# Optimization experiments

Hardware: AMD Instinct MI355X
Metric: run time of the kernel (lower is better)

## Reference

```python
import jax, jax.numpy as jnp
import numpy as np

OUT_F, IN_F = 4096, 4096
TOKENS = 8192


def setup_inputs() -> dict:
    key = jax.random.key(0)
    k0, k1, k2, k3 = jax.random.split(key, 4)
    CORE_SCALE = 0.05  # keep reconstructed W finite and well below the 1e6 sanity bound
    x = jax.random.normal(k0, (TOKENS, IN_F), dtype=jnp.float32)
    core0 = jax.random.normal(k1, (1, 16, 16, 64), dtype=jnp.float32) * CORE_SCALE
    core1 = jax.random.normal(k2, (64, 16, 16, 64), dtype=jnp.float32) * CORE_SCALE
    core2 = jax.random.normal(k3, (64, 16, 16, 1), dtype=jnp.float32) * CORE_SCALE
    return {"x": x, "core0": core0, "core1": core1, "core2": core2}


def _build_weight(cores):
    # Chain tensordot over bond dims: cores[k] is [r_{k-1}, o_k, i_k, r_k]
    t = cores[0].astype(jnp.float32)
    for c in cores[1:]:
        t = jnp.tensordot(t, c.astype(jnp.float32), axes=((-1,), (0,)))
    # squeeze the boundary bonds (both 1 for open boundary)
    t = t[0, ..., 0]  # shape [o1, i1, o2, i2, o3, i3]
    num = len(cores)
    # order 'oi': all o-axes first, then all i-axes (matches _contract_4d_chain_with)
    perm = list(range(0, 2 * num, 2)) + list(range(1, 2 * num, 2))
    t = jnp.transpose(t, perm)
    W = t.reshape(OUT_F, IN_F)
    # _clean_finite: nan/inf -> 0 (identity on finite values)
    return jnp.nan_to_num(W, nan=0.0, posinf=0.0, neginf=0.0)


def reference(x, core0, core1, core2):
    W = _build_weight([core0, core1, core2])  # [out_f, in_f], fp32
    # dense path: y = x @ W^T (nn.Linear semantics, no bias)
    return jnp.matmul(x, W.T)
```

## Files before the change

kernel.cpp:

```cpp
#include <hip/hip_runtime.h>

typedef __attribute__((ext_vector_type(8))) short  s8v;
typedef __attribute__((ext_vector_type(8))) unsigned short us8;
typedef __attribute__((ext_vector_type(4))) unsigned short us4;
typedef __attribute__((ext_vector_type(4))) float  f4v;

__device__ __forceinline__ unsigned short f2bf(float f) {
  unsigned int u = __builtin_bit_cast(unsigned int, f);
  u += 0x7fffu + ((u >> 16) & 1u);
  return (unsigned short)(u >> 16);
}

__device__ __forceinline__ void gll16(const void* g, void* l) {
  __builtin_amdgcn_global_load_lds(
      (const __attribute__((address_space(1))) unsigned int*)g,
      (__attribute__((address_space(3))) unsigned int*)l, 16, 0, 0);
}

__global__ __launch_bounds__(256) void cast_bf16(const float* __restrict__ in,
                                                 unsigned short* __restrict__ out) {
  const size_t i = (size_t)blockIdx.x * 256 + threadIdx.x;
  const f4v* p = (const f4v*)in;
  f4v a = p[2 * i];
  f4v b = p[2 * i + 1];
  us8 r;
  r[0] = f2bf(a[0]); r[1] = f2bf(a[1]); r[2] = f2bf(a[2]); r[3] = f2bf(a[3]);
  r[4] = f2bf(b[0]); r[5] = f2bf(b[1]); r[6] = f2bf(b[2]); r[7] = f2bf(b[3]);
  *(us8*)&out[i * 8] = r;
}

__global__ __launch_bounds__(256) void contract1b(const float* __restrict__ c0,
                                                  const float* __restrict__ c1,
                                                  unsigned short* __restrict__ T) {
  const int idx = blockIdx.x * 256 + threadIdx.x;
  const int r2q = idx & 15;
  const int oi2 = (idx >> 4) & 255;
  const int oi1 = idx >> 12;
  const float* c0p = c0 + oi1 * 64;
  const float* c1p = c1 + oi2 * 64 + r2q * 4;
  f4v s = (f4v)0.f;
#pragma unroll 8
  for (int r1 = 0; r1 < 64; ++r1) {
    const float t = c0p[r1];
    const f4v v = *(const f4v*)(c1p + r1 * 16384);
    s[0] = fmaf(t, v[0], s[0]); s[1] = fmaf(t, v[1], s[1]);
    s[2] = fmaf(t, v[2], s[2]); s[3] = fmaf(t, v[3], s[3]);
  }
  us4 o;
  o[0] = f2bf(s[0]); o[1] = f2bf(s[1]); o[2] = f2bf(s[2]); o[3] = f2bf(s[3]);
  *(us4*)&T[(size_t)idx * 4] = o;
}

__global__ __launch_bounds__(256) void transc2(const float* __restrict__ c2,
                                               unsigned short* __restrict__ c2t) {
  const int n = blockIdx.x * 16 + (threadIdx.x >> 4);
  const int j = threadIdx.x & 15;
  us4 o;
#pragma unroll
  for (int q = 0; q < 4; ++q) o[q] = f2bf(c2[(j * 4 + q) * 256 + n]);
  *(us4*)&c2t[(size_t)n * 64 + j * 4] = o;
}

__global__ __launch_bounds__(256) void buildW3(const unsigned short* __restrict__ T,
                                               const unsigned short* __restrict__ c2t,
                                               unsigned short* __restrict__ W) {
  __shared__ unsigned short sT[16384];
  __shared__ unsigned short sC[16384];

  const int tid = threadIdx.x;
  const int o1 = blockIdx.x >> 4, o2 = blockIdx.x & 15;

#pragma unroll
  for (int j = 0; j < 8; ++j) {
    const int c = j * 256 + tid;
    const int m = c >> 3, sl = c & 7;
    const int dst = m * 64 + ((sl ^ (m & 7)) << 3);
    *(us8*)&sT[dst] = *(const us8*)(T + (size_t)(o1 * 16 + (m >> 4)) * 16384 +
                                    (o2 * 16 + (m & 15)) * 64 + sl * 8);
    *(us8*)&sC[dst] = *(const us8*)(c2t + (size_t)m * 64 + sl * 8);
  }
  __syncthreads();

  const int lane = tid & 63, wid = tid >> 6;
  const int fr = lane & 15, ks = lane >> 4;
  const int f7 = fr & 7;
  const int sx0 = ((ks ^ f7) << 3);
  const int sx1 = (((4 + ks) ^ f7) << 3);

  s8v a[4][2];
#pragma unroll
  for (int mi = 0; mi < 4; ++mi) {
    const unsigned short* p = &sT[(wid * 64 + mi * 16 + fr) * 64];
    a[mi][0] = *(const s8v*)(p + sx0);
    a[mi][1] = *(const s8v*)(p + sx1);
  }
#pragma unroll
  for (int nt = 0; nt < 16; ++nt) {
    const unsigned short* p = &sC[(nt * 16 + fr) * 64];
    const s8v b0 = *(const s8v*)(p + sx0);
    const s8v b1 = *(const s8v*)(p + sx1);
#pragma unroll
    for (int mi = 0; mi < 4; ++mi) {
      f4v acc = (f4v)0.f;
      acc = __builtin_amdgcn_mfma_f32_16x16x32_bf16(a[mi][0], b0, acc, 0, 0, 0);
      acc = __builtin_amdgcn_mfma_f32_16x16x32_bf16(a[mi][1], b1, acc, 0, 0, 0);
      unsigned short* wp = W + (size_t)(o1 * 256 + o2 * 16 + nt) * 4096 +
                           (wid * 4 + mi) * 256 + fr;
#pragma unroll
      for (int r = 0; r < 4; ++r) wp[(ks * 4 + r) * 16] = f2bf(acc[r]);
    }
  }
}


#define BAR() __builtin_amdgcn_s_barrier()
#define VMW(N) asm volatile("s_waitcnt vmcnt(" #N ")" ::: "memory")

template<int MQ, int NQ>
__device__ __forceinline__ void mmq(f4v (&acc)[8][4], const s8v (&a)[4][2], const s8v (&b)[2][2]) {
  __builtin_amdgcn_s_setprio(1);
#pragma unroll
  for (int mi = 0; mi < 4; ++mi)
#pragma unroll
    for (int ni = 0; ni < 2; ++ni)
#pragma unroll
      for (int q = 0; q < 2; ++q)
        acc[MQ * 4 + mi][NQ * 2 + ni] = __builtin_amdgcn_mfma_f32_16x16x32_bf16(
            a[mi][q], b[ni][q], acc[MQ * 4 + mi][NQ * 2 + ni], 0, 0, 0);
  __builtin_amdgcn_s_setprio(0);
}

__global__ __launch_bounds__(512, 2) void gemm8(const unsigned short* __restrict__ A,
                                                const unsigned short* __restrict__ B,
                                                float* __restrict__ C) {
  constexpr int M = 8192, N = 4096, K = 4096;
  constexpr int NT = K / 64;
  constexpr int NITER = NT / 2;
  constexpr int NXT = N / 256;

  __shared__ unsigned short lds[65536];

  const int tid  = threadIdx.x;
  const int lane = tid & 63;
  const int wid  = tid >> 6;
  const int wm   = wid >> 2;
  const int wn   = wid & 3;

  const int cpx = (int)gridDim.x >> 3;
  const int wg  = ((int)blockIdx.x & 7) * cpx + ((int)blockIdx.x >> 3);
  const long bm = (long)(wg / NXT) * 256;
  const long bn = (long)(wg % NXT) * 256;

  const int srow = tid >> 3;
  const int scol = ((tid & 7) ^ (srow & 7)) * 8;
  const unsigned short* gA = A + (bm + srow) * (size_t)K + scol;
  const unsigned short* gB = B + (bn + srow) * (size_t)K + scol;
  const size_t half64 = 64 * (size_t)K;
  const size_t k128   = 128 * (size_t)K;

#define STG(gp, koff, ldsU) do {                                  \
    const unsigned short* g_ = (gp) + (koff);                     \
    gll16(g_,          &lds[(ldsU) + tid * 8]);                   \
    gll16(g_ + half64, &lds[(ldsU) + 4096 + tid * 8]);            \
  } while (0)

  const int fr = lane & 15;
  const int ks = lane >> 4;
  const int f7 = fr & 7;
  const int sx0 = (ks ^ f7) * 8;
  const int sx1 = ((ks | 4) ^ f7) * 8;
  const int arow = (wm * 64 + fr) * 64;
  const int brow = (wn * 32 + fr) * 64;

#define RDA(MQ, bufU) do {                                                   \
    const unsigned short* p_ = &lds[(bufU) + (MQ) * 8192 + arow];            \
    a[0][0] = *(const s8v*)(p_ + sx0);        a[0][1] = *(const s8v*)(p_ + sx1); \
    a[1][0] = *(const s8v*)(p_ + 1024 + sx0); a[1][1] = *(const s8v*)(p_ + 1024 + sx1); \
    a[2][0] = *(const s8v*)(p_ + 2048 + sx0); a[2][1] = *(const s8v*)(p_ + 2048 + sx1); \
    a[3][0] = *(const s8v*)(p_ + 3072 + sx0); a[3][1] = *(const s8v*)(p_ + 3072 + sx1); \
  } while (0)
#define RDB(dst, NQ, bufU) do {                                              \
    const unsigned short* p_ = &lds[(bufU) + 16384 + (NQ) * 8192 + brow];    \
    dst[0][0] = *(const s8v*)(p_ + sx0);        dst[0][1] = *(const s8v*)(p_ + sx1); \
    dst[1][0] = *(const s8v*)(p_ + 1024 + sx0); dst[1][1] = *(const s8v*)(p_ + 1024 + sx1); \
  } while (0)

  f4v acc[8][4];
#pragma unroll
  for (int m = 0; m < 8; ++m)
#pragma unroll
    for (int n = 0; n < 4; ++n) acc[m][n] = (f4v)0.0f;

  STG(gA,        0, 0);
  STG(gA + k128, 0, 8192);
  STG(gB,        0, 16384);
  STG(gB + k128, 0, 24576);
  STG(gA,        64, 32768);
  STG(gB + k128, 64, 32768 + 24576);
  VMW(4);
  BAR();

  s8v a[4][2], bL[2][2], bH[2][2];

  for (int i = 0; i < NITER; ++i) {
    const long w = (i == NITER - 1) ? -4096L : 0L;
    RDA(0, 0); RDB(bL, 0, 0); RDB(bH, 1, 0);
    STG(gA + k128, 64, 32768 + 8192);
    BAR(); mmq<0, 0>(acc, a, bL); BAR();
    STG(gB, 64, 32768 + 16384);
    BAR(); mmq<0, 1>(acc, a, bH); BAR();
    RDA(1, 0);
    STG(gA, 128 + w, 0);
    BAR(); mmq<1, 1>(acc, a, bH); BAR();
    STG(gB + k128, 128 + w, 24576);
    BAR(); mmq<1, 0>(acc, a, bL);
    VMW(4); BAR();
    RDA(0, 32768); RDB(bL, 0, 32768); RDB(bH, 1, 32768);
    STG(gA + k128, 128 + w, 8192);
    BAR(); mmq<0, 0>(acc, a, bL); BAR();
    STG(gB, 128 + w, 16384);
    BAR(); mmq<0, 1>(acc, a, bH); BAR();
    RDA(1, 32768);
    STG(gA, 192 + w, 32768);
    BAR(); mmq<1, 1>(acc, a, bH); BAR();
    STG(gB + k128, 192 + w, 32768 + 24576);
    BAR(); mmq<1, 0>(acc, a, bL);
    VMW(4); BAR();

    gA += 128; gB += 128;
  }
  VMW(0);

#pragma unroll
  for (int mq = 0; mq < 2; ++mq)
#pragma unroll
    for (int mi = 0; mi < 4; ++mi)
#pragma unroll
      for (int nq = 0; nq < 2; ++nq)
#pragma unroll
        for (int ni = 0; ni < 2; ++ni) {
          const size_t row0 = bm + mq * 128 + wm * 64 + mi * 16 + ks * 4;
          const size_t col  = bn + nq * 128 + wn * 32 + ni * 16 + fr;
          float* cp = C + row0 * (size_t)N + col;
          f4v v = acc[mq * 4 + mi][nq * 2 + ni];
          cp[0] = v[0]; cp[N] = v[1]; cp[2 * (size_t)N] = v[2]; cp[3 * (size_t)N] = v[3];
        }
#undef STG
#undef RDA
#undef RDB
}

extern "C" void kernel_launch(void* const* d_in, const int* in_sizes, int n_in,
                              void* d_out, int out_size, void* d_ws, size_t ws_size,
                              hipStream_t stream) {
  const float* x  = (const float*)d_in[0];
  const float* c0 = (const float*)d_in[1];
  const float* c1 = (const float*)d_in[2];
  const float* c2 = (const float*)d_in[3];
  float* out = (float*)d_out;

  char* ws = (char*)d_ws;
  unsigned short* T   = (unsigned short*)ws;
  unsigned short* c2t = (unsigned short*)(ws + (8u << 20));
  unsigned short* Wb  = (unsigned short*)(ws + (16u << 20));
  unsigned short* xb  = (unsigned short*)(ws + (48u << 20));

  hipLaunchKernelGGL(cast_bf16,  dim3(16384), dim3(256), 0, stream, x, xb);
  hipLaunchKernelGGL(contract1b, dim3(4096),  dim3(256), 0, stream, c0, c1, T);
  hipLaunchKernelGGL(transc2,    dim3(16),    dim3(256), 0, stream, c2, c2t);
  hipLaunchKernelGGL(buildW3,    dim3(256),   dim3(256), 0, stream, T, c2t, Wb);
  hipLaunchKernelGGL(gemm8,      dim3(512),   dim3(512), 0, stream, xb, Wb, out);
}
```

Baseline: 313.5 us.

## Replace 256x256 ping-pong GEMM with 128x256 triple-buffered K=32 pipeline

Replaces the hand-scheduled 256x256-tile GEMM, which interleaves its barriers and MFMA quarters with a K=64 double buffer, with a simpler 128x256 tile kernel. The new kernel uses K=32 steps and a three-stage LDS ring buffer, 72KB in total. Occupancy is raised (launch bounds 4 blocks/CU, 1024 blocks), which trades the old intra-block staggering for cross-block latency hiding. Smaller M tiles mean more global traffic for B and more barriers per unit of work.

```diff
diff --git a/kernel.cpp b/kernel.cpp
--- a/kernel.cpp
+++ b/kernel.cpp
@@ -116,29 +116,14 @@
 #define BAR() __builtin_amdgcn_s_barrier()
 #define VMW(N) asm volatile("s_waitcnt vmcnt(" #N ")" ::: "memory")
 
-template<int MQ, int NQ>
-__device__ __forceinline__ void mmq(f4v (&acc)[8][4], const s8v (&a)[4][2], const s8v (&b)[2][2]) {
-  __builtin_amdgcn_s_setprio(1);
-#pragma unroll
-  for (int mi = 0; mi < 4; ++mi)
-#pragma unroll
-    for (int ni = 0; ni < 2; ++ni)
-#pragma unroll
-      for (int q = 0; q < 2; ++q)
-        acc[MQ * 4 + mi][NQ * 2 + ni] = __builtin_amdgcn_mfma_f32_16x16x32_bf16(
-            a[mi][q], b[ni][q], acc[MQ * 4 + mi][NQ * 2 + ni], 0, 0, 0);
-  __builtin_amdgcn_s_setprio(0);
-}
-
-__global__ __launch_bounds__(512, 2) void gemm8(const unsigned short* __restrict__ A,
+__global__ __launch_bounds__(512, 4) void gemmq(const unsigned short* __restrict__ A,
                                                 const unsigned short* __restrict__ B,
                                                 float* __restrict__ C) {
-  constexpr int M = 8192, N = 4096, K = 4096;
-  constexpr int NT = K / 64;
-  constexpr int NITER = NT / 2;
+  constexpr int N = 4096, K = 4096;
+  constexpr int NKT = K / 32;
   constexpr int NXT = N / 256;
 
-  __shared__ unsigned short lds[65536];
+  __shared__ unsigned short lds[36864];
 
   const int tid  = threadIdx.x;
   const int lane = tid & 63;
@@ -148,106 +133,76 @@
 
   const int cpx = (int)gridDim.x >> 3;
   const int wg  = ((int)blockIdx.x & 7) * cpx + ((int)blockIdx.x >> 3);
-  const long bm = (long)(wg / NXT) * 256;
+  const long bm = (long)(wg / NXT) * 128;
   const long bn = (long)(wg % NXT) * 256;
 
-  const int srow = tid >> 3;
-  const int scol = ((tid & 7) ^ (srow & 7)) * 8;
+  const int srow = tid >> 2;
+  const int scol = ((tid & 3) ^ ((srow >> 1) & 3)) * 8;
   const unsigned short* gA = A + (bm + srow) * (size_t)K + scol;
   const unsigned short* gB = B + (bn + srow) * (size_t)K + scol;
-  const size_t half64 = 64 * (size_t)K;
-  const size_t k128   = 128 * (size_t)K;
-
-#define STG(gp, koff, ldsU) do {                                  \
-    const unsigned short* g_ = (gp) + (koff);                     \
-    gll16(g_,          &lds[(ldsU) + tid * 8]);                   \
-    gll16(g_ + half64, &lds[(ldsU) + 4096 + tid * 8]);            \
+  const size_t b128off = 128 * (size_t)K;
+
+#define STG(koff, bufU) do {                                        \
+    gll16(gA + (koff),           &lds[(bufU) + tid * 8]);           \
+    gll16(gB + (koff),           &lds[(bufU) + 4096 + tid * 8]);    \
+    gll16(gB + b128off + (koff), &lds[(bufU) + 8192 + tid * 8]);    \
   } while (0)
 
   const int fr = lane & 15;
   const int ks = lane >> 4;
-  const int f7 = fr & 7;
-  const int sx0 = (ks ^ f7) * 8;
-  const int sx1 = ((ks | 4) ^ f7) * 8;
-  const int arow = (wm * 64 + fr) * 64;
-  const int brow = (wn * 32 + fr) * 64;
-
-#define RDA(MQ, bufU) do {                                                   \
-    const unsigned short* p_ = &lds[(bufU) + (MQ) * 8192 + arow];            \
-    a[0][0] = *(const s8v*)(p_ + sx0);        a[0][1] = *(const s8v*)(p_ + sx1); \
-    a[1][0] = *(const s8v*)(p_ + 1024 + sx0); a[1][1] = *(const s8v*)(p_ + 1024 + sx1); \
-    a[2][0] = *(const s8v*)(p_ + 2048 + sx0); a[2][1] = *(const s8v*)(p_ + 2048 + sx1); \
-    a[3][0] = *(const s8v*)(p_ + 3072 + sx0); a[3][1] = *(const s8v*)(p_ + 3072 + sx1); \
-  } while (0)
-#define RDB(dst, NQ, bufU) do {                                              \
-    const unsigned short* p_ = &lds[(bufU) + 16384 + (NQ) * 8192 + brow];    \
-    dst[0][0] = *(const s8v*)(p_ + sx0);        dst[0][1] = *(const s8v*)(p_ + sx1); \
-    dst[1][0] = *(const s8v*)(p_ + 1024 + sx0); dst[1][1] = *(const s8v*)(p_ + 1024 + sx1); \
-  } while (0)
-
-  f4v acc[8][4];
-#pragma unroll
-  for (int m = 0; m < 8; ++m)
+  const int swz = (ks ^ ((fr >> 1) & 3)) * 8;
+  const int aoff = (wm * 64 + fr) * 32 + swz;
+  const int boff = 4096 + (wn * 64 + fr) * 32 + swz;
+
+  f4v acc[4][4];
+#pragma unroll
+  for (int m = 0; m < 4; ++m)
 #pragma unroll
     for (int n = 0; n < 4; ++n) acc[m][n] = (f4v)0.0f;
 
-  STG(gA,        0, 0);
-  STG(gA + k128, 0, 8192);
-  STG(gB,        0, 16384);
-  STG(gB + k128, 0, 24576);
-  STG(gA,        64, 32768);
-  STG(gB + k128, 64, 32768 + 24576);
-  VMW(4);
+  STG(0, 0);
+  STG(32, 12288);
+  VMW(3);
   BAR();
 
-  s8v a[4][2], bL[2][2], bH[2][2];
-
-  for (int i = 0; i < NITER; ++i) {
-    const long w = (i == NITER - 1) ? -4096L : 0L;
-    RDA(0, 0); RDB(bL, 0, 0); RDB(bH, 1, 0);
-    STG(gA + k128, 64, 32768 + 8192);
-    BAR(); mmq<0, 0>(acc, a, bL); BAR();
-    STG(gB, 64, 32768 + 16384);
-    BAR(); mmq<0, 1>(acc, a, bH); BAR();
-    RDA(1, 0);
-    STG(gA, 128 + w, 0);
-    BAR(); mmq<1, 1>(acc, a, bH); BAR();
-    STG(gB + k128, 128 + w, 24576);
-    BAR(); mmq<1, 0>(acc, a, bL);
-    VMW(4); BAR();
-    RDA(0, 32768); RDB(bL, 0, 32768); RDB(bH, 1, 32768);
-    STG(gA + k128, 128 + w, 8192);
-    BAR(); mmq<0, 0>(acc, a, bL); BAR();
-    STG(gB, 128 + w, 16384);
-    BAR(); mmq<0, 1>(acc, a, bH); BAR();
-    RDA(1, 32768);
-    STG(gA, 192 + w, 32768);
-    BAR(); mmq<1, 1>(acc, a, bH); BAR();
-    STG(gB + k128, 192 + w, 32768 + 24576);
-    BAR(); mmq<1, 0>(acc, a, bL);
-    VMW(4); BAR();
-
-    gA += 128; gB += 128;
+  int cu = 0, nx = 12288, s2 = 24576;
+
+  for (int t = 0; t < NKT; ++t) {
+    const int koff = (t < NKT - 2) ? (t + 2) * 32 : 0;
+    STG(koff, s2);
+    VMW(3);
+    BAR();
+
+    s8v a[4], b[4];
+#pragma unroll
+    for (int mf = 0; mf < 4; ++mf) a[mf] = *(const s8v*)&lds[cu + aoff + mf * 512];
+#pragma unroll
+    for (int nf = 0; nf < 4; ++nf) b[nf] = *(const s8v*)&lds[cu + boff + nf * 512];
+
+    __builtin_amdgcn_s_setprio(1);
+#pragma unroll
+    for (int mf = 0; mf < 4; ++mf)
+#pragma unroll
+      for (int nf = 0; nf < 4; ++nf)
+        acc[mf][nf] = __builtin_amdgcn_mfma_f32_16x16x32_bf16(a[mf], b[nf], acc[mf][nf], 0, 0, 0);
+    __builtin_amdgcn_s_setprio(0);
+    BAR();
+
+    const int tmp = s2; s2 = cu; cu = nx; nx = tmp;
   }
   VMW(0);
 
-#pragma unroll
-  for (int mq = 0; mq < 2; ++mq)
-#pragma unroll
-    for (int mi = 0; mi < 4; ++mi)
-#pragma unroll
-      for (int nq = 0; nq < 2; ++nq)
-#pragma unroll
-        for (int ni = 0; ni < 2; ++ni) {
-          const size_t row0 = bm + mq * 128 + wm * 64 + mi * 16 + ks * 4;
-          const size_t col  = bn + nq * 128 + wn * 32 + ni * 16 + fr;
-          float* cp = C + row0 * (size_t)N + col;
-          f4v v = acc[mq * 4 + mi][nq * 2 + ni];
-          cp[0] = v[0]; cp[N] = v[1]; cp[2 * (size_t)N] = v[2]; cp[3 * (size_t)N] = v[3];
-        }
+  const size_t crow0 = bm + wm * 64 + ks * 4;
+  const size_t ccol0 = bn + wn * 64 + fr;
+#pragma unroll
+  for (int mf = 0; mf < 4; ++mf)
+#pragma unroll
+    for (int nf = 0; nf < 4; ++nf) {
+      float* cp = C + (crow0 + mf * 16) * (size_t)N + ccol0 + nf * 16;
+      f4v v = acc[mf][nf];
+      cp[0] = v[0]; cp[N] = v[1]; cp[2 * (size_t)N] = v[2]; cp[3 * (size_t)N] = v[3];
+    }
 #undef STG
-#undef RDA
-#undef RDB
 }
 
 extern "C" void kernel_launch(void* const* d_in, const int* in_sizes, int n_in,
@@ -269,5 +224,5 @@
   hipLaunchKernelGGL(contract1b, dim3(4096),  dim3(256), 0, stream, c0, c1, T);
   hipLaunchKernelGGL(transc2,    dim3(16),    dim3(256), 0, stream, c2, c2t);
   hipLaunchKernelGGL(buildW3,    dim3(256),   dim3(256), 0, stream, T, c2t, Wb);
-  hipLaunchKernelGGL(gemm8,      dim3(512),   dim3(512), 0, stream, xb, Wb, out);
-}
+  hipLaunchKernelGGL(gemmq,      dim3(1024),  dim3(512), 0, stream, xb, Wb, out);
+}
```

Result: slower. 373.4 us (+19.1%).

## Reschedule GEMM prefetch pipeline with fewer barriers and reordered staging

Applied to the files above, without the earlier changes.

Restructures the main GEMM loop's software pipeline. Global-to-LDS stage loads are reordered and regrouped, and the MFMA quadrant order changes so bL/bH halves are reused differently. About half of the workgroup barriers around each MFMA block are removed, and the vmcnt wait drops from 4 to 2. The barrier macro now carries compiler memory fences. The aim is less synchronisation stall and better overlap of loads with compute, at the risk of LDS races or wrong wraparound offsets on the last iteration.

```diff
diff --git a/kernel.cpp b/kernel.cpp
--- a/kernel.cpp
+++ b/kernel.cpp
@@ -113,7 +113,7 @@
 }
 
 
-#define BAR() __builtin_amdgcn_s_barrier()
+#define SBAR() do { asm volatile("" ::: "memory"); __builtin_amdgcn_s_barrier(); asm volatile("" ::: "memory"); } while (0)
 #define VMW(N) asm volatile("s_waitcnt vmcnt(" #N ")" ::: "memory")
 
 template<int MQ, int NQ>
@@ -133,7 +133,7 @@
 __global__ __launch_bounds__(512, 2) void gemm8(const unsigned short* __restrict__ A,
                                                 const unsigned short* __restrict__ B,
                                                 float* __restrict__ C) {
-  constexpr int M = 8192, N = 4096, K = 4096;
+  constexpr int N = 4096, K = 4096;
   constexpr int NT = K / 64;
   constexpr int NITER = NT / 2;
   constexpr int NXT = N / 256;
@@ -196,36 +196,36 @@
   STG(gB,        0, 16384);
   STG(gB + k128, 0, 24576);
   STG(gA,        64, 32768);
-  STG(gB + k128, 64, 32768 + 24576);
-  VMW(4);
-  BAR();
+  VMW(2);
+  SBAR();
 
   s8v a[4][2], bL[2][2], bH[2][2];
 
   for (int i = 0; i < NITER; ++i) {
-    const long w = (i == NITER - 1) ? -4096L : 0L;
+    const long w46 = (i == NITER - 1) ? -128L : 0L;
+    const long w8  = (i == NITER - 1) ? -192L : 0L;
     RDA(0, 0); RDB(bL, 0, 0); RDB(bH, 1, 0);
+    STG(gB, 64, 32768 + 16384);
+    SBAR(); mmq<0, 0>(acc, a, bL);
     STG(gA + k128, 64, 32768 + 8192);
-    BAR(); mmq<0, 0>(acc, a, bL); BAR();
-    STG(gB, 64, 32768 + 16384);
-    BAR(); mmq<0, 1>(acc, a, bH); BAR();
+    STG(gB + k128, 64, 32768 + 24576);
+    SBAR(); mmq<0, 1>(acc, a, bH);
     RDA(1, 0);
-    STG(gA, 128 + w, 0);
-    BAR(); mmq<1, 1>(acc, a, bH); BAR();
-    STG(gB + k128, 128 + w, 24576);
-    BAR(); mmq<1, 0>(acc, a, bL);
-    VMW(4); BAR();
+    SBAR(); mmq<1, 0>(acc, a, bL);
+    STG(gA, 128 + w46, 0);
+    SBAR(); mmq<1, 1>(acc, a, bH);
+    VMW(2); SBAR();
     RDA(0, 32768); RDB(bL, 0, 32768); RDB(bH, 1, 32768);
-    STG(gA + k128, 128 + w, 8192);
-    BAR(); mmq<0, 0>(acc, a, bL); BAR();
-    STG(gB, 128 + w, 16384);
-    BAR(); mmq<0, 1>(acc, a, bH); BAR();
+    STG(gB, 128 + w46, 16384);
+    SBAR(); mmq<0, 0>(acc, a, bL);
+    STG(gA + k128, 128 + w46, 8192);
+    STG(gB + k128, 128 + w46, 24576);
+    SBAR(); mmq<0, 1>(acc, a, bH);
     RDA(1, 32768);
-    STG(gA, 192 + w, 32768);
-    BAR(); mmq<1, 1>(acc, a, bH); BAR();
-    STG(gB + k128, 192 + w, 32768 + 24576);
-    BAR(); mmq<1, 0>(acc, a, bL);
-    VMW(4); BAR();
+    SBAR(); mmq<1, 0>(acc, a, bL);
+    STG(gA, 192 + w8, 32768);
+    SBAR(); mmq<1, 1>(acc, a, bH);
+    VMW(2); SBAR();
 
     gA += 128; gB += 128;
   }
```

Result: faster. 306.9 us (-2.1%).

## Double-buffer A/B register fragments and reorder GEMM main-loop stages

Applied to the files above, without the earlier changes.

Restructures the bf16 GEMM main loop to keep two A fragments and two B fragments in registers. Each LDS read is now issued ahead of the MFMA block that consumes it, and the per-stage double barriers around each MFMA block are removed. The global-to-LDS staging order and the last-iteration wraparound offsets are reworked to match. Holding more fragments live raises register pressure under launch_bounds(512,2), and the changed barrier placement must still protect LDS buffer reuse.

```diff
diff --git a/kernel.cpp b/kernel.cpp
--- a/kernel.cpp
+++ b/kernel.cpp
@@ -133,7 +133,7 @@
 __global__ __launch_bounds__(512, 2) void gemm8(const unsigned short* __restrict__ A,
                                                 const unsigned short* __restrict__ B,
                                                 float* __restrict__ C) {
-  constexpr int M = 8192, N = 4096, K = 4096;
+  constexpr int N = 4096, K = 4096;
   constexpr int NT = K / 64;
   constexpr int NITER = NT / 2;
   constexpr int NXT = N / 256;
@@ -172,12 +172,12 @@
   const int arow = (wm * 64 + fr) * 64;
   const int brow = (wn * 32 + fr) * 64;
 
-#define RDA(MQ, bufU) do {                                                   \
+#define RDA(dst, MQ, bufU) do {                                              \
     const unsigned short* p_ = &lds[(bufU) + (MQ) * 8192 + arow];            \
-    a[0][0] = *(const s8v*)(p_ + sx0);        a[0][1] = *(const s8v*)(p_ + sx1); \
-    a[1][0] = *(const s8v*)(p_ + 1024 + sx0); a[1][1] = *(const s8v*)(p_ + 1024 + sx1); \
-    a[2][0] = *(const s8v*)(p_ + 2048 + sx0); a[2][1] = *(const s8v*)(p_ + 2048 + sx1); \
-    a[3][0] = *(const s8v*)(p_ + 3072 + sx0); a[3][1] = *(const s8v*)(p_ + 3072 + sx1); \
+    dst[0][0] = *(const s8v*)(p_ + sx0);        dst[0][1] = *(const s8v*)(p_ + sx1); \
+    dst[1][0] = *(const s8v*)(p_ + 1024 + sx0); dst[1][1] = *(const s8v*)(p_ + 1024 + sx1); \
+    dst[2][0] = *(const s8v*)(p_ + 2048 + sx0); dst[2][1] = *(const s8v*)(p_ + 2048 + sx1); \
+    dst[3][0] = *(const s8v*)(p_ + 3072 + sx0); dst[3][1] = *(const s8v*)(p_ + 3072 + sx1); \
   } while (0)
 #define RDB(dst, NQ, bufU) do {                                              \
     const unsigned short* p_ = &lds[(bufU) + 16384 + (NQ) * 8192 + brow];    \
@@ -196,36 +196,53 @@
   STG(gB,        0, 16384);
   STG(gB + k128, 0, 24576);
   STG(gA,        64, 32768);
-  STG(gB + k128, 64, 32768 + 24576);
-  VMW(4);
+  STG(gB,        64, 32768 + 16384);
+  STG(gA + k128, 64, 32768 + 8192);
+  VMW(6);
   BAR();
 
-  s8v a[4][2], bL[2][2], bH[2][2];
+  s8v a0[4][2], a1[4][2], b0[2][2], b1[2][2];
+  RDA(a0, 0, 0);
+  RDB(b0, 0, 0);
+  BAR();
 
   for (int i = 0; i < NITER; ++i) {
-    const long w = (i == NITER - 1) ? -4096L : 0L;
-    RDA(0, 0); RDB(bL, 0, 0); RDB(bH, 1, 0);
-    STG(gA + k128, 64, 32768 + 8192);
-    BAR(); mmq<0, 0>(acc, a, bL); BAR();
-    STG(gB, 64, 32768 + 16384);
-    BAR(); mmq<0, 1>(acc, a, bH); BAR();
-    RDA(1, 0);
-    STG(gA, 128 + w, 0);
-    BAR(); mmq<1, 1>(acc, a, bH); BAR();
-    STG(gB + k128, 128 + w, 24576);
-    BAR(); mmq<1, 0>(acc, a, bL);
+    const long w2 = (i == NITER - 1) ? -128L : 0L;
+    const long w3 = (i == NITER - 1) ? -192L : 0L;
+    RDA(a1, 1, 0);
+    STG(gB + k128, 64, 32768 + 24576);
+    mmq<0, 0>(acc, a0, b0);
+    BAR();
+    RDB(b1, 1, 0);
+    STG(gA, 128 + w2, 0);
+    mmq<1, 0>(acc, a1, b0);
+    BAR();
+    STG(gB, 128 + w2, 16384);
+    mmq<1, 1>(acc, a1, b1);
+    BAR();
+    STG(gA + k128, 128 + w2, 8192);
+    mmq<0, 1>(acc, a0, b1);
     VMW(4); BAR();
-    RDA(0, 32768); RDB(bL, 0, 32768); RDB(bH, 1, 32768);
-    STG(gA + k128, 128 + w, 8192);
-    BAR(); mmq<0, 0>(acc, a, bL); BAR();
-    STG(gB, 128 + w, 16384);
-    BAR(); mmq<0, 1>(acc, a, bH); BAR();
-    RDA(1, 32768);
-    STG(gA, 192 + w, 32768);
-    BAR(); mmq<1, 1>(acc, a, bH); BAR();
-    STG(gB + k128, 192 + w, 32768 + 24576);
-    BAR(); mmq<1, 0>(acc, a, bL);
+    RDA(a0, 0, 32768);
+    RDB(b0, 0, 32768);
+    BAR();
+    RDA(a1, 1, 32768);
+    STG(gB + k128, 128 + w2, 24576);
+    mmq<0, 0>(acc, a0, b0);
+    BAR();
+    RDB(b1, 1, 32768);
+    STG(gA, 192 + w3, 32768);
+    mmq<1, 0>(acc, a1, b0);
+    BAR();
+    STG(gB, 192 + w3, 32768 + 16384);
+    mmq<1, 1>(acc, a1, b1);
+    BAR();
+    STG(gA + k128, 192 + w3, 32768 + 8192);
+    mmq<0, 1>(acc, a0, b1);
     VMW(4); BAR();
+    RDA(a0, 0, 0);
+    RDB(b0, 0, 0);
+    BAR();
 
     gA += 128; gB += 128;
   }
```

New measurement: 320.2 us. 1.02x slower.
